# Optimization experiments

Hardware: AMD Instinct MI355X
Metric: run time of the kernel (lower is better)

Reference implementation:

```python
import jax, jax.numpy as jnp
import numpy as np

NUM_HEADS = 16
D_MODEL = 1024
D_K = D_MODEL // NUM_HEADS
MAX_SEQ_LEN = 4096
ROPE_BASE = 10000.0
BATCH = 2
SEQ_LEN = 2048


def _rope_tables(seq_len, d_k, base=ROPE_BASE):
    # theta_i = 1 / base^(2i/d_k), i = 0..d_k/2-1
    theta = 1.0 / base ** (jnp.arange(0, d_k, 2, dtype=jnp.float32) / d_k)
    m = jnp.arange(seq_len, dtype=jnp.float32)
    m_theta = jnp.outer(m, theta)                      # [S, d_k/2]
    ang = jnp.concatenate([m_theta, m_theta], axis=-1)  # [S, d_k]
    return jnp.cos(ang), jnp.sin(ang)


def _apply_rope(x, cos, sin):
    # x: [B, H, S, d_k]; rotate-half: cat(-x2, x1)
    d2 = x.shape[-1] // 2
    x1, x2 = x[..., :d2], x[..., d2:]
    x_flip = jnp.concatenate([-x2, x1], axis=-1)
    return x * cos + x_flip * sin


def setup_inputs() -> dict:
    key = jax.random.key(0)
    kx, kq, kk, kv, ko = jax.random.split(key, 5)
    s = 1.0 / np.sqrt(D_MODEL)  # ~ nn.Linear default init scale
    x = jax.random.normal(kx, (BATCH, SEQ_LEN, D_MODEL), dtype=jnp.float32)
    W_Q = jax.random.uniform(kq, (D_MODEL, D_MODEL), jnp.float32, -s, s)
    W_K = jax.random.uniform(kk, (D_MODEL, D_MODEL), jnp.float32, -s, s)
    W_V = jax.random.uniform(kv, (D_MODEL, D_MODEL), jnp.float32, -s, s)
    W_O = jax.random.uniform(ko, (D_MODEL, D_MODEL), jnp.float32, -s, s)
    return {"x": x, "W_Q": W_Q, "W_K": W_K, "W_V": W_V, "W_O": W_O}


def reference(x, W_Q, W_K, W_V, W_O):
    B, S, _ = x.shape
    # Linear with weight [out, in]: y = x @ W.T
    def proj(W):
        y = jnp.einsum('bsd,ed->bse', x, W)
        return y.reshape(B, S, NUM_HEADS, D_K).transpose(0, 2, 1, 3)  # [B,H,S,dk]
    Q, K, V = proj(W_Q), proj(W_K), proj(W_V)
    cos, sin = _rope_tables(S, D_K)
    Q = _apply_rope(Q, cos, sin)
    K = _apply_rope(K, cos, sin)
    scores = jnp.einsum('bhsd,bhtd->bhst', Q, K) / jnp.sqrt(jnp.float32(D_K))
    causal = jnp.tril(jnp.ones((S, S), dtype=bool))
    scores = jnp.where(causal[None, None], scores, -jnp.inf)
    attn = jax.nn.softmax(scores, axis=-1)
    out = jnp.einsum('bhst,bhtd->bhsd', attn, V)
    out = out.transpose(0, 2, 1, 3).reshape(B, S, D_MODEL)
    return jnp.einsum('bsd,ed->bse', out, W_O)
```

## Files before the change

### kernel.cpp

```cpp
#include <hip/hip_runtime.h>
#include <hip/hip_bf16.h>

#define BATCH 2
#define SEQ 2048
#define DM 1024
#define NH 16
#define DKH 64

typedef __attribute__((ext_vector_type(8))) __bf16 bf16x8;
typedef __attribute__((ext_vector_type(4))) float f32x4;
typedef __attribute__((ext_vector_type(2))) float f32x2;
typedef __attribute__((ext_vector_type(8))) unsigned short ushort8;

__device__ __forceinline__ void gload16(const void* g, void* l) {
  __builtin_amdgcn_global_load_lds(
      (const __attribute__((address_space(1))) void*)g,
      (__attribute__((address_space(3))) void*)l, 16, 0, 0);
}

__global__ void cast_x(const float* __restrict__ in, __bf16* __restrict__ out) {
  int i = blockIdx.x * blockDim.x + threadIdx.x;
  f32x4 a = ((const f32x4*)in)[2 * i], b = ((const f32x4*)in)[2 * i + 1];
  bf16x8 o;
  o[0]=(__bf16)a[0]; o[1]=(__bf16)a[1]; o[2]=(__bf16)a[2]; o[3]=(__bf16)a[3];
  o[4]=(__bf16)b[0]; o[5]=(__bf16)b[1]; o[6]=(__bf16)b[2]; o[7]=(__bf16)b[3];
  ((bf16x8*)out)[i] = o;
}

__global__ void cast_w(const float* __restrict__ w0, const float* __restrict__ w1,
                       const float* __restrict__ w2, const float* __restrict__ w3,
                       __bf16* __restrict__ out) {
  const float* src = (blockIdx.y == 0) ? w0 : (blockIdx.y == 1) ? w1
                   : (blockIdx.y == 2) ? w2 : w3;
  __bf16* dst = out + (size_t)blockIdx.y * (DM * DM);
  int i = blockIdx.x * blockDim.x + threadIdx.x;
  f32x4 a = ((const f32x4*)src)[2 * i], b = ((const f32x4*)src)[2 * i + 1];
  bf16x8 o;
  o[0]=(__bf16)a[0]; o[1]=(__bf16)a[1]; o[2]=(__bf16)a[2]; o[3]=(__bf16)a[3];
  o[4]=(__bf16)b[0]; o[5]=(__bf16)b[1]; o[6]=(__bf16)b[2]; o[7]=(__bf16)b[3];
  ((bf16x8*)dst)[i] = o;
}

__global__ void gen_tab(float* __restrict__ tab) {
  int idx = blockIdx.x * blockDim.x + threadIdx.x;
  int s = idx >> 5, i = idx & 31;
  float theta = exp2f((float)i * -0.41524101186092029f);
  float sn, c;
  sincosf((float)s * theta, &sn, &c);
  tab[2 * idx] = c;
  tab[2 * idx + 1] = sn;
}

#define QSCALE 0.1803368801111137f

template<int EPI, int BN>
__launch_bounds__(256, 3)
__global__ void gemm_bt(const __bf16* __restrict__ A, const __bf16* __restrict__ B,
                        void* __restrict__ Cout, int M, int N, int K,
                        const float* __restrict__ tab) {
  __shared__ __bf16 As[128 * 64];
  __shared__ __bf16 Bs[BN * 64];
  const int tid = threadIdx.x;
  const int lane = tid & 63;
  const int w = tid >> 6;
  const int wr = w >> 1, wc = w & 1;
  const int fr = lane & 15, fq = lane >> 4;
  const int m0 = blockIdx.x * 128;
  const int n0 = blockIdx.y * BN;
  const int NFR = BN / 32;

  f32x4 acc[4][BN / 32] = {};
  const int NT = K >> 6;

  for (int kt = 0; kt < NT; ++kt) {
    const int k0 = kt << 6;
    __syncthreads();
    #pragma unroll
    for (int p = 0; p < 4; ++p) {
      int c = p * 256 + tid;
      int row = c >> 3, cs = (c & 7) ^ (row & 7);
      gload16(&A[(size_t)(m0 + row) * K + k0 + cs * 8], &As[(p * 256 + w * 64) * 8]);
    }
    #pragma unroll
    for (int p = 0; p < BN / 32; ++p) {
      int c = p * 256 + tid;
      int row = c >> 3, cs = (c & 7) ^ (row & 7);
      gload16(&B[(size_t)(n0 + row) * K + k0 + cs * 8], &Bs[(p * 256 + w * 64) * 8]);
    }
    __syncthreads();
    #pragma unroll
    for (int kk = 0; kk < 2; ++kk) {
      bf16x8 af[4], bfr[BN / 32];
      #pragma unroll
      for (int mf = 0; mf < 4; ++mf) {
        int row = wr * 64 + mf * 16 + fr;
        af[mf] = *(const bf16x8*)&As[row * 64 + ((kk * 32 + fq * 8) ^ ((fr & 7) << 3))];
      }
      #pragma unroll
      for (int nf = 0; nf < NFR; ++nf) {
        int row = wc * (BN / 2) + nf * 16 + fr;
        bfr[nf] = *(const bf16x8*)&Bs[row * 64 + ((kk * 32 + fq * 8) ^ ((fr & 7) << 3))];
      }
      __builtin_amdgcn_s_setprio(1);
      #pragma unroll
      for (int mf = 0; mf < 4; ++mf)
        #pragma unroll
        for (int nf = 0; nf < NFR; ++nf)
          acc[mf][nf] = __builtin_amdgcn_mfma_f32_16x16x32_bf16(af[mf], bfr[nf], acc[mf][nf], 0, 0, 0);
      __builtin_amdgcn_s_setprio(0);
    }
  }

  if (EPI == 0) {
    const int nbase = n0 + wc * 64;
    const int which = nbase >> 10;
    const int h = (nbase & 1023) >> 6;
    const int b = m0 >> 11;
    __bf16* base0 = (__bf16*)Cout + (size_t)which * (4u << 20);
    if (which < 2) {
      const float scale = (which == 0) ? QSCALE : 1.0f;
      __bf16* dst = base0 + ((size_t)(b * NH + h)) * SEQ * DKH;
      #pragma unroll
      for (int mf = 0; mf < 4; ++mf) {
        #pragma unroll
        for (int j = 0; j < 4; ++j) {
          int s = (m0 & (SEQ - 1)) + wr * 64 + mf * 16 + fq * 4 + j;
          #pragma unroll
          for (int nf = 0; nf < 2; ++nf) {
            int i = nf * 16 + fr;
            f32x2 cs = ((const f32x2*)tab)[s * 32 + i];
            float a = acc[mf][nf][j], bb = acc[mf][nf + 2][j];
            dst[(size_t)s * DKH + i]      = (__bf16)((a * cs[0] - bb * cs[1]) * scale);
            dst[(size_t)s * DKH + i + 32] = (__bf16)((bb * cs[0] + a * cs[1]) * scale);
          }
        }
      }
    } else {
      __bf16* dst = base0 + ((size_t)(b * NH + h)) * DKH * SEQ;
      #pragma unroll
      for (int mf = 0; mf < 4; ++mf) {
        #pragma unroll
        for (int nf = 0; nf < 4; ++nf) {
          int dk = nf * 16 + fr;
          #pragma unroll
          for (int j = 0; j < 4; ++j) {
            int sp = (m0 & (SEQ - 1)) + wr * 64 + (mf >> 1) * 32 + fq * 8 + (mf & 1) * 4 + j;
            dst[(size_t)dk * SEQ + sp] = (__bf16)acc[mf][nf][j];
          }
        }
      }
    }
  } else {
    #pragma unroll
    for (int mf = 0; mf < 4; ++mf)
      #pragma unroll
      for (int nf = 0; nf < NFR; ++nf)
        #pragma unroll
        for (int j = 0; j < 4; ++j) {
          int m = m0 + wr * 64 + mf * 16 + fq * 4 + j;
          int n = n0 + wc * (BN / 2) + nf * 16 + fr;
          ((float*)Cout)[(size_t)m * N + n] = acc[mf][nf][j];
        }
  }
}

__launch_bounds__(512, 4)
__global__ void attn_causal(const __bf16* __restrict__ Qg, const __bf16* __restrict__ Kg,
                            const __bf16* __restrict__ Vtg, __bf16* __restrict__ Out,
                            float* __restrict__ P0, float* __restrict__ P1,
                            float* __restrict__ L0, float* __restrict__ L1) {
  __shared__ __bf16 Ks[2][64 * 64];
  __shared__ __bf16 Vts[2][64 * 64];
  const int tid = threadIdx.x;
  const int lane = tid & 63;
  const int w = tid >> 6;
  const int fr = lane & 15, fq = lane >> 4;
  const int bid = blockIdx.x;
  const int bh = bid >> 4;
  const int slot = bid & 15;
  const bool isA = slot < 8;
  const int qa = slot;
  const int qb = isA ? (15 - slot) : slot;
  const int sw  = isA ? (2 * qa + 2) : 99;
  const int off = isA ? (15 - 2 * qa) : 0;
  const int b = bh >> 4, h = bh & 15;
  const __bf16* Qh = Qg + (size_t)bh * SEQ * DKH;
  const __bf16* Kh = Kg + (size_t)bh * SEQ * DKH;
  const __bf16* Vth = Vtg + (size_t)bh * DKH * SEQ;

  int qrow_lo = (isA ? qa : qb) * 128 + w * 16;

  bf16x8 qf[2];
  #pragma unroll
  for (int kk = 0; kk < 2; ++kk)
    qf[kk] = *(const bf16x8*)&Qh[(size_t)(qrow_lo + fr) * DKH + kk * 32 + fq * 8];

  f32x4 Oa[4] = {};
  float lsum = 0.f;

  {
    int cch = w * 64 + lane;
    int row = cch >> 3, cs = (cch & 7) ^ (row & 7);
    gload16(&Kh[(size_t)row * DKH + cs * 8], &Ks[0][(w * 64) * 8]);
    gload16(&Vth[(size_t)row * SEQ + cs * 8], &Vts[0][(w * 64) * 8]);
  }
  __syncthreads();

  for (int it = 0; it < 17; ++it) {
    const int cur = it & 1;
    if (it + 1 < 17) {
      const int nx = it + 1;
      const int kvn = (nx < sw) ? nx : nx + off;
      const int tn = kvn << 6;
      int cch = w * 64 + lane;
      int row = cch >> 3, cs = (cch & 7) ^ (row & 7);
      gload16(&Kh[(size_t)(tn + row) * DKH + cs * 8], &Ks[cur ^ 1][(w * 64) * 8]);
      gload16(&Vth[(size_t)row * SEQ + tn + cs * 8], &Vts[cur ^ 1][(w * 64) * 8]);
    }
    if (isA && it == sw) {
      float ls = lsum;
      ls += __shfl_xor(ls, 16);
      ls += __shfl_xor(ls, 32);
      float rl[4];
      #pragma unroll
      for (int j = 0; j < 4; ++j)
        rl[j] = 1.0f / __shfl(ls, fq * 4 + j);
      #pragma unroll
      for (int nf = 0; nf < 4; ++nf)
        #pragma unroll
        for (int j = 0; j < 4; ++j) {
          int qr = qrow_lo + fq * 4 + j;
          Out[((size_t)(b * SEQ) + qr) * DM + h * DKH + nf * 16 + fr] =
              (__bf16)(Oa[nf][j] * rl[j]);
        }
      #pragma unroll
      for (int nf = 0; nf < 4; ++nf) Oa[nf] = (f32x4){0.f, 0.f, 0.f, 0.f};
      lsum = 0.f;
      qrow_lo = qb * 128 + w * 16;
      #pragma unroll
      for (int kk = 0; kk < 2; ++kk)
        qf[kk] = *(const bf16x8*)&Qh[(size_t)(qrow_lo + fr) * DKH + kk * 32 + fq * 8];
    }
    const int kvt = (it < sw) ? it : it + off;
    const int ts = kvt << 6;
    if (ts <= qrow_lo + 15) {
      f32x4 sacc[4] = {};
      __builtin_amdgcn_s_setprio(1);
      #pragma unroll
      for (int kk = 0; kk < 2; ++kk) {
        #pragma unroll
        for (int nf = 0; nf < 4; ++nf) {
          int krow = nf * 16 + fr;
          bf16x8 kf = *(const bf16x8*)&Ks[cur][krow * 64 + ((kk * 32 + fq * 8) ^ ((fr & 7) << 3))];
          sacc[nf] = __builtin_amdgcn_mfma_f32_16x16x32_bf16(kf, qf[kk], sacc[nf], 0, 0, 0);
        }
      }
      __builtin_amdgcn_s_setprio(0);
      const bool need_mask = (ts + 63 > qrow_lo);
      const int qr = qrow_lo + fr;
      #pragma unroll
      for (int nf = 0; nf < 4; ++nf) {
        #pragma unroll
        for (int j = 0; j < 4; ++j) {
          float v = sacc[nf][j];
          if (need_mask) {
            int tc = ts + nf * 16 + fq * 4 + j;
            if (tc > qr) v = -INFINITY;
          }
          float pv = exp2f(v);
          lsum += pv;
          sacc[nf][j] = pv;
        }
      }
      bf16x8 pa[2];
      #pragma unroll
      for (int kk = 0; kk < 2; ++kk)
        #pragma unroll
        for (int e = 0; e < 8; ++e)
          pa[kk][e] = (__bf16)sacc[2 * kk + (e >> 2)][e & 3];
      __builtin_amdgcn_s_setprio(1);
      #pragma unroll
      for (int kk = 0; kk < 2; ++kk) {
        #pragma unroll
        for (int nf = 0; nf < 4; ++nf) {
          int d = nf * 16 + fr;
          bf16x8 vf = *(const bf16x8*)&Vts[cur][d * 64 + ((kk * 32 + fq * 8) ^ ((fr & 7) << 3))];
          Oa[nf] = __builtin_amdgcn_mfma_f32_16x16x32_bf16(pa[kk], vf, Oa[nf], 0, 0, 0);
        }
      }
      __builtin_amdgcn_s_setprio(0);
    }
    __syncthreads();
  }
  float* P = isA ? P1 : P0;
  float* L = isA ? L1 : L0;
  const int rbase = ((bh << 3) + (qb - 8)) << 7;
  float ls = lsum;
  ls += __shfl_xor(ls, 16);
  ls += __shfl_xor(ls, 32);
  if (lane < 16) L[rbase + w * 16 + lane] = ls;
  #pragma unroll
  for (int nf = 0; nf < 4; ++nf)
    #pragma unroll
    for (int j = 0; j < 4; ++j)
      P[(size_t)(rbase + w * 16 + fq * 4 + j) * 64 + nf * 16 + fr] = Oa[nf][j];
}

__global__ void combine(const float* __restrict__ P0, const float* __restrict__ P1,
                        const float* __restrict__ L0, const float* __restrict__ L1,
                        __bf16* __restrict__ Ab) {
  int t = blockIdx.x * blockDim.x + threadIdx.x;
  int rowid = t >> 3, d0 = (t & 7) * 8;
  int bh = rowid >> 10, rem = rowid & 1023;
  int tq = rem >> 7, r = rem & 127;
  float rl = 1.0f / (L0[rowid] + L1[rowid]);
  const float* p0 = P0 + (size_t)rowid * 64 + d0;
  const float* p1 = P1 + (size_t)rowid * 64 + d0;
  f32x4 a0 = *(const f32x4*)p0, a1 = *(const f32x4*)(p0 + 4);
  f32x4 b0 = *(const f32x4*)p1, b1 = *(const f32x4*)(p1 + 4);
  bf16x8 o;
  #pragma unroll
  for (int e = 0; e < 4; ++e) {
    o[e]     = (__bf16)((a0[e] + b0[e]) * rl);
    o[e + 4] = (__bf16)((a1[e] + b1[e]) * rl);
  }
  int s = (tq + 8) * 128 + r;
  int b = bh >> 4, h = bh & 15;
  *(bf16x8*)&Ab[((size_t)b * SEQ + s) * DM + h * DKH + d0] = o;
}

extern "C" void kernel_launch(void* const* d_in, const int* in_sizes, int n_in,
                              void* d_out, int out_size, void* d_ws, size_t ws_size,
                              hipStream_t stream) {
  const float* x  = (const float*)d_in[0];
  const float* Wq = (const float*)d_in[1];
  const float* Wk = (const float*)d_in[2];
  const float* Wv = (const float*)d_in[3];
  const float* Wo = (const float*)d_in[4];

  char* ws = (char*)d_ws;
  __bf16* xb  = (__bf16*)(ws);
  __bf16* wqb = (__bf16*)(ws + ( 8u << 20));
  __bf16* wob = (__bf16*)(ws + (14u << 20));
  __bf16* Qb  = (__bf16*)(ws + (16u << 20));
  __bf16* Kb  = (__bf16*)(ws + (24u << 20));
  __bf16* Vtb = (__bf16*)(ws + (32u << 20));
  __bf16* Ab  = (__bf16*)(ws + (40u << 20));
  float*  tab = (float*)(ws + (48u << 20));
  float*  L0  = (float*)(ws + (49u << 20));
  float*  L1  = (float*)(ws + (49u << 20) + (1u << 18));
  float* P0 = (float*)d_out;
  float* P1 = P0 + (32768 * 64);

  cast_x<<<dim3(2048), dim3(256), 0, stream>>>(x, xb);
  cast_w<<<dim3(512, 4), dim3(256), 0, stream>>>(Wq, Wk, Wv, Wo, wqb);
  gen_tab<<<dim3(256), dim3(256), 0, stream>>>(tab);

  gemm_bt<0, 128><<<dim3(32, 24), dim3(256), 0, stream>>>(xb, wqb, Qb, BATCH * SEQ, 3 * DM, DM, tab);

  attn_causal<<<dim3(512), dim3(512), 0, stream>>>(Qb, Kb, Vtb, Ab, P0, P1, L0, L1);

  combine<<<dim3(1024), dim3(256), 0, stream>>>(P0, P1, L0, L1, Ab);

  gemm_bt<1, 64><<<dim3(32, 16), dim3(256), 0, stream>>>(Ab, wob, d_out, BATCH * SEQ, DM, DM, nullptr);
}
```

Measured before the change: 104.4 us.

## Process two 16-row query groups per wave in causal attention to reuse K/V fragments

Result: slower. 115.0 us (+10.2%).

```diff
diff --git a/kernel.cpp b/kernel.cpp
--- a/kernel.cpp
+++ b/kernel.cpp
@@ -164,7 +164,7 @@
   }
 }
 
-__launch_bounds__(512, 4)
+__launch_bounds__(256, 4)
 __global__ void attn_causal(const __bf16* __restrict__ Qg, const __bf16* __restrict__ Kg,
                             const __bf16* __restrict__ Vtg, __bf16* __restrict__ Out,
                             float* __restrict__ P0, float* __restrict__ P1,
@@ -188,21 +188,24 @@
   const __bf16* Kh = Kg + (size_t)bh * SEQ * DKH;
   const __bf16* Vth = Vtg + (size_t)bh * DKH * SEQ;
 
-  int qrow_lo = (isA ? qa : qb) * 128 + w * 16;
-
-  bf16x8 qf[2];
+  int qrow0 = (isA ? qa : qb) * 128 + w * 32;
+
+  bf16x8 qf[2][2];
   #pragma unroll
-  for (int kk = 0; kk < 2; ++kk)
-    qf[kk] = *(const bf16x8*)&Qh[(size_t)(qrow_lo + fr) * DKH + kk * 32 + fq * 8];
-
-  f32x4 Oa[4] = {};
-  float lsum = 0.f;
-
-  {
-    int cch = w * 64 + lane;
-    int row = cch >> 3, cs = (cch & 7) ^ (row & 7);
-    gload16(&Kh[(size_t)row * DKH + cs * 8], &Ks[0][(w * 64) * 8]);
-    gload16(&Vth[(size_t)row * SEQ + cs * 8], &Vts[0][(w * 64) * 8]);
+  for (int g = 0; g < 2; ++g)
+    #pragma unroll
+    for (int kk = 0; kk < 2; ++kk)
+      qf[g][kk] = *(const bf16x8*)&Qh[(size_t)(qrow0 + g * 16 + fr) * DKH + kk * 32 + fq * 8];
+
+  f32x4 Oa0[4] = {}, Oa1[4] = {};
+  float lsum0 = 0.f, lsum1 = 0.f;
+
+  #pragma unroll
+  for (int p = 0; p < 2; ++p) {
+    int c = p * 256 + tid;
+    int row = c >> 3, cs = (c & 7) ^ (row & 7);
+    gload16(&Kh[(size_t)row * DKH + cs * 8], &Ks[0][(p * 256 + w * 64) * 8]);
+    gload16(&Vth[(size_t)row * SEQ + cs * 8], &Vts[0][(p * 256 + w * 64) * 8]);
   }
   __syncthreads();
 
@@ -212,39 +215,51 @@
       const int nx = it + 1;
       const int kvn = (nx < sw) ? nx : nx + off;
       const int tn = kvn << 6;
-      int cch = w * 64 + lane;
-      int row = cch >> 3, cs = (cch & 7) ^ (row & 7);
-      gload16(&Kh[(size_t)(tn + row) * DKH + cs * 8], &Ks[cur ^ 1][(w * 64) * 8]);
-      gload16(&Vth[(size_t)row * SEQ + tn + cs * 8], &Vts[cur ^ 1][(w * 64) * 8]);
+      #pragma unroll
+      for (int p = 0; p < 2; ++p) {
+        int c = p * 256 + tid;
+        int row = c >> 3, cs = (c & 7) ^ (row & 7);
+        gload16(&Kh[(size_t)(tn + row) * DKH + cs * 8], &Ks[cur ^ 1][(p * 256 + w * 64) * 8]);
+        gload16(&Vth[(size_t)row * SEQ + tn + cs * 8], &Vts[cur ^ 1][(p * 256 + w * 64) * 8]);
+      }
     }
     if (isA && it == sw) {
-      float ls = lsum;
-      ls += __shfl_xor(ls, 16);
-      ls += __shfl_xor(ls, 32);
-      float rl[4];
-      #pragma unroll
-      for (int j = 0; j < 4; ++j)
-        rl[j] = 1.0f / __shfl(ls, fq * 4 + j);
-      #pragma unroll
-      for (int nf = 0; nf < 4; ++nf)
-        #pragma unroll
-        for (int j = 0; j < 4; ++j) {
-          int qr = qrow_lo + fq * 4 + j;
-          Out[((size_t)(b * SEQ) + qr) * DM + h * DKH + nf * 16 + fr] =
-              (__bf16)(Oa[nf][j] * rl[j]);
-        }
-      #pragma unroll
-      for (int nf = 0; nf < 4; ++nf) Oa[nf] = (f32x4){0.f, 0.f, 0.f, 0.f};
-      lsum = 0.f;
-      qrow_lo = qb * 128 + w * 16;
-      #pragma unroll
-      for (int kk = 0; kk < 2; ++kk)
-        qf[kk] = *(const bf16x8*)&Qh[(size_t)(qrow_lo + fr) * DKH + kk * 32 + fq * 8];
+      #pragma unroll
+      for (int g = 0; g < 2; ++g) {
+        float ls = g ? lsum1 : lsum0;
+        ls += __shfl_xor(ls, 16);
+        ls += __shfl_xor(ls, 32);
+        float rl[4];
+        #pragma unroll
+        for (int j = 0; j < 4; ++j)
+          rl[j] = 1.0f / __shfl(ls, fq * 4 + j);
+        #pragma unroll
+        for (int nf = 0; nf < 4; ++nf)
+          #pragma unroll
+          for (int j = 0; j < 4; ++j) {
+            int qr = qrow0 + g * 16 + fq * 4 + j;
+            float ov = g ? Oa1[nf][j] : Oa0[nf][j];
+            Out[((size_t)(b * SEQ) + qr) * DM + h * DKH + nf * 16 + fr] =
+                (__bf16)(ov * rl[j]);
+          }
+      }
+      #pragma unroll
+      for (int nf = 0; nf < 4; ++nf) {
+        Oa0[nf] = (f32x4){0.f, 0.f, 0.f, 0.f};
+        Oa1[nf] = (f32x4){0.f, 0.f, 0.f, 0.f};
+      }
+      lsum0 = lsum1 = 0.f;
+      qrow0 = qb * 128 + w * 32;
+      #pragma unroll
+      for (int g = 0; g < 2; ++g)
+        #pragma unroll
+        for (int kk = 0; kk < 2; ++kk)
+          qf[g][kk] = *(const bf16x8*)&Qh[(size_t)(qrow0 + g * 16 + fr) * DKH + kk * 32 + fq * 8];
     }
     const int kvt = (it < sw) ? it : it + off;
     const int ts = kvt << 6;
-    if (ts <= qrow_lo + 15) {
-      f32x4 sacc[4] = {};
+    if (ts <= qrow0 + 31) {
+      f32x4 s0[4] = {}, s1[4] = {};
       __builtin_amdgcn_s_setprio(1);
       #pragma unroll
       for (int kk = 0; kk < 2; ++kk) {
@@ -252,32 +267,36 @@
         for (int nf = 0; nf < 4; ++nf) {
           int krow = nf * 16 + fr;
           bf16x8 kf = *(const bf16x8*)&Ks[cur][krow * 64 + ((kk * 32 + fq * 8) ^ ((fr & 7) << 3))];
-          sacc[nf] = __builtin_amdgcn_mfma_f32_16x16x32_bf16(kf, qf[kk], sacc[nf], 0, 0, 0);
+          s0[nf] = __builtin_amdgcn_mfma_f32_16x16x32_bf16(kf, qf[0][kk], s0[nf], 0, 0, 0);
+          s1[nf] = __builtin_amdgcn_mfma_f32_16x16x32_bf16(kf, qf[1][kk], s1[nf], 0, 0, 0);
         }
       }
       __builtin_amdgcn_s_setprio(0);
-      const bool need_mask = (ts + 63 > qrow_lo);
-      const int qr = qrow_lo + fr;
+      const int qr0 = qrow0 + fr;
+      const int qr1 = qrow0 + 16 + fr;
+      const bool m0_ = (ts + 63 > qrow0);
+      const bool m1_ = (ts + 63 > qrow0 + 16);
       #pragma unroll
       for (int nf = 0; nf < 4; ++nf) {
         #pragma unroll
         for (int j = 0; j < 4; ++j) {
-          float v = sacc[nf][j];
-          if (need_mask) {
-            int tc = ts + nf * 16 + fq * 4 + j;
-            if (tc > qr) v = -INFINITY;
-          }
-          float pv = exp2f(v);
-          lsum += pv;
-          sacc[nf][j] = pv;
-        }
-      }
-      bf16x8 pa[2];
+          int tc = ts + nf * 16 + fq * 4 + j;
+          float v0 = s0[nf][j], v1 = s1[nf][j];
+          if (m0_ && tc > qr0) v0 = -INFINITY;
+          if (m1_ && tc > qr1) v1 = -INFINITY;
+          float p0 = exp2f(v0), p1 = exp2f(v1);
+          lsum0 += p0; lsum1 += p1;
+          s0[nf][j] = p0; s1[nf][j] = p1;
+        }
+      }
+      bf16x8 pa0[2], pa1[2];
       #pragma unroll
       for (int kk = 0; kk < 2; ++kk)
         #pragma unroll
-        for (int e = 0; e < 8; ++e)
-          pa[kk][e] = (__bf16)sacc[2 * kk + (e >> 2)][e & 3];
+        for (int e = 0; e < 8; ++e) {
+          pa0[kk][e] = (__bf16)s0[2 * kk + (e >> 2)][e & 3];
+          pa1[kk][e] = (__bf16)s1[2 * kk + (e >> 2)][e & 3];
+        }
       __builtin_amdgcn_s_setprio(1);
       #pragma unroll
       for (int kk = 0; kk < 2; ++kk) {
@@ -285,7 +304,8 @@
         for (int nf = 0; nf < 4; ++nf) {
           int d = nf * 16 + fr;
           bf16x8 vf = *(const bf16x8*)&Vts[cur][d * 64 + ((kk * 32 + fq * 8) ^ ((fr & 7) << 3))];
-          Oa[nf] = __builtin_amdgcn_mfma_f32_16x16x32_bf16(pa[kk], vf, Oa[nf], 0, 0, 0);
+          Oa0[nf] = __builtin_amdgcn_mfma_f32_16x16x32_bf16(pa0[kk], vf, Oa0[nf], 0, 0, 0);
+          Oa1[nf] = __builtin_amdgcn_mfma_f32_16x16x32_bf16(pa1[kk], vf, Oa1[nf], 0, 0, 0);
         }
       }
       __builtin_amdgcn_s_setprio(0);
@@ -294,16 +314,21 @@
   }
   float* P = isA ? P1 : P0;
   float* L = isA ? L1 : L0;
-  const int rbase = ((bh << 3) + (qb - 8)) << 7;
-  float ls = lsum;
-  ls += __shfl_xor(ls, 16);
-  ls += __shfl_xor(ls, 32);
-  if (lane < 16) L[rbase + w * 16 + lane] = ls;
+  const int rbase = (((bh << 3) + (qb - 8)) << 7) + w * 32;
   #pragma unroll
-  for (int nf = 0; nf < 4; ++nf)
-    #pragma unroll
-    for (int j = 0; j < 4; ++j)
-      P[(size_t)(rbase + w * 16 + fq * 4 + j) * 64 + nf * 16 + fr] = Oa[nf][j];
+  for (int g = 0; g < 2; ++g) {
+    float ls = g ? lsum1 : lsum0;
+    ls += __shfl_xor(ls, 16);
+    ls += __shfl_xor(ls, 32);
+    if (lane < 16) L[rbase + g * 16 + lane] = ls;
+    #pragma unroll
+    for (int nf = 0; nf < 4; ++nf)
+      #pragma unroll
+      for (int j = 0; j < 4; ++j) {
+        float ov = g ? Oa1[nf][j] : Oa0[nf][j];
+        P[(size_t)(rbase + g * 16 + fq * 4 + j) * 64 + nf * 16 + fr] = ov;
+      }
+  }
 }
 
 __global__ void combine(const float* __restrict__ P0, const float* __restrict__ P1,
@@ -358,7 +383,7 @@
 
   gemm_bt<0, 128><<<dim3(32, 24), dim3(256), 0, stream>>>(xb, wqb, Qb, BATCH * SEQ, 3 * DM, DM, tab);
 
-  attn_causal<<<dim3(512), dim3(512), 0, stream>>>(Qb, Kb, Vtb, Ab, P0, P1, L0, L1);
+  attn_causal<<<dim3(512), dim3(256), 0, stream>>>(Qb, Kb, Vtb, Ab, P0, P1, L0, L1);
 
   combine<<<dim3(1024), dim3(256), 0, stream>>>(P0, P1, L0, L1, Ab);
 
```
